# Performance work log

Measured on AMD Instinct MI355X. Metric: run time of the kernel, lower is better.

Reference implementation:

```python
import jax, jax.numpy as jnp
import numpy as np

TOP_K = 2  # init arg top_k
EPS = 1e-9


def setup_inputs() -> dict:
    key = jax.random.key(0)
    ks = jax.random.split(key, 5)
    B, L, D, E, H, G = 2, 2048, 2048, 8, 2048, 256
    s = lambda k, sh, fan: jax.random.normal(k, sh, jnp.float32) / np.sqrt(fan)
    return {
        "x": jax.random.normal(ks[0], (B, L, D), jnp.float32),
        "wg1": s(ks[1], (D, G), D),
        "wg2": s(ks[2], (G, E), G),
        "w1": s(ks[3], (E, D, H), D),
        "w2": s(ks[4], (E, H, D), H),
    }


def reference(x, wg1, wg2, w1, w2):
    B, L, D = x.shape
    xf = x.reshape(-1, D)                                  # [T, D]
    T = xf.shape[0]

    # --- top-k gating (mlp gate) ---
    logits = jax.nn.gelu(xf @ wg1) @ wg2                   # [T, E]
    probs = jax.nn.softmax(logits, axis=-1)                # [T, E]
    top_vals, top_idx = jax.lax.top_k(probs, TOP_K)        # [T, k]
    # dense gate matrix: gate weight where expert selected, else 0
    gates = jnp.zeros_like(probs).at[jnp.arange(T)[:, None], top_idx].set(top_vals)  # [T, E]

    # --- grouped expert FFN (dense-equivalent of gather/grouped-GEMM/scatter) ---
    h = jax.nn.gelu(jnp.einsum('td,edh->teh', xf, w1))     # [T, E, H]
    gh = h * gates[:, :, None]                             # fold gates in (linear in h)
    y = jnp.einsum('teh,ehd->td', gh, w2).reshape(B, L, D)

    # --- mutual-information aux loss: -H(E) + H(E|X) ---
    p_mean = probs.mean(axis=0)                            # [E]
    loss = jnp.sum(p_mean * jnp.log(p_mean + EPS)) \
         - jnp.mean(jnp.sum(probs * jnp.log(probs + EPS), axis=-1))
    return y, loss
```

## Files before the change

kernel.cpp:

```cpp
#include <hip/hip_runtime.h>

#define T_TOK 4096
#define NROWS_MAX 10240
#define MAX_TILES 40

typedef float  fv4  __attribute__((ext_vector_type(4)));
typedef __bf16 bv4  __attribute__((ext_vector_type(4)));
typedef __bf16 bv8  __attribute__((ext_vector_type(8)));

#define CTRL_OFF     0
#define ROWTOK_OFF   4096
#define ROWGATE_OFF  45056
#define TOPIDX_OFF   86016
#define TOPVAL_OFF   118784
#define G_OFF        151552
#define XB_OFF       4345856
#define W1T_OFF      21123072
#define W2T_OFF      88231936
#define HBUF_OFF     155340800

struct Ctrl {
    int   counts[8];
    float psum[8];
    float entsum;
    int   ntiles;
    int   off[8];
    int   tile_e[MAX_TILES];
    int   tile_r0[MAX_TILES];
};

__device__ __forceinline__ float gelu_f(float x) {
    float x3 = x * x * x;
    return 0.5f * x * (1.0f + tanhf(0.7978845608028654f * (x + 0.044715f * x3)));
}

__device__ __forceinline__ void g2l16(const void* gptr, void* lptr) {
    __builtin_amdgcn_global_load_lds(
        (const __attribute__((address_space(1))) void*)gptr,
        (__attribute__((address_space(3))) void*)lptr, 16, 0, 0);
}

__global__ __launch_bounds__(256) void transpose_cvt(
    const float* __restrict__ w1, const float* __restrict__ w2,
    __bf16* __restrict__ w1t, __bf16* __restrict__ w2t)
{
    int b    = blockIdx.x;
    int mat  = b >> 10;
    int tile = b & 1023;
    int trow = tile >> 5, tcol = tile & 31;
    const float* src = (mat < 8) ? (w1 + (size_t)mat * 4194304)
                                 : (w2 + (size_t)(mat - 8) * 4194304);
    __bf16* dst = (mat < 8) ? (w1t + (size_t)mat * 4194304)
                            : (w2t + (size_t)(mat - 8) * 4194304);
    __shared__ float tileS[64][65];
    int tid = threadIdx.x;
    int c = tid & 63, r4 = tid >> 6;
#pragma unroll
    for (int u = 0; u < 16; u++) {
        int rr = u * 4 + r4;
        tileS[rr][c] = src[(size_t)(trow * 64 + rr) * 2048 + tcol * 64 + c];
    }
    __syncthreads();
    int c2 = (tid & 31) * 2, r8 = tid >> 5;
#pragma unroll
    for (int u = 0; u < 8; u++) {
        int rr = u * 8 + r8;
        __bf16 v0 = (__bf16)tileS[c2][rr];
        __bf16 v1 = (__bf16)tileS[c2 + 1][rr];
        size_t o = (size_t)(tcol * 64 + rr) * 2048 + trow * 64 + c2;
        dst[o]     = v0;
        dst[o + 1] = v1;
    }
}

__global__ __launch_bounds__(256) void cvt_x_kernel(const float* __restrict__ x,
                                                    __bf16* __restrict__ xb)
{
    size_t idx = ((size_t)blockIdx.x * 256 + threadIdx.x) * 4;
    fv4 v = *(const fv4*)(x + idx);
    bv4 o;
#pragma unroll
    for (int u = 0; u < 4; u++) o[u] = (__bf16)v[u];
    *(bv4*)(xb + idx) = o;
}

__global__ __launch_bounds__(256) void gating_gemm(const float* __restrict__ x,
                                                   const float* __restrict__ wg1,
                                                   float* __restrict__ g)
{
    __shared__ float As[16][68];
    __shared__ float Bs[16][68];
    int tid = threadIdx.x;
    int tx = tid & 15, ty = tid >> 4;
    int mb = blockIdx.x, nb = blockIdx.y;
    float acc[4][4];
#pragma unroll
    for (int u = 0; u < 4; u++)
#pragma unroll
        for (int v = 0; v < 4; v++) acc[u][v] = 0.f;

    int r  = tid >> 2, kq = tid & 3;
    int kb = tid >> 4, n4 = (tid & 15) * 4;
    const float* gx = x + (size_t)(mb * 64 + r) * 2048 + kq * 4;
    const float* gw = wg1 + nb * 64 + n4;

    for (int k0 = 0; k0 < 2048; k0 += 16) {
        fv4 av = *(const fv4*)(gx + k0);
        fv4 bv = *(const fv4*)(gw + (size_t)(k0 + kb) * 256);
        __syncthreads();
#pragma unroll
        for (int u = 0; u < 4; u++) As[kq * 4 + u][r] = av[u];
        *(fv4*)&Bs[kb][n4] = bv;
        __syncthreads();
#pragma unroll
        for (int k = 0; k < 16; k++) {
            fv4 a = *(const fv4*)&As[k][ty * 4];
            fv4 b = *(const fv4*)&Bs[k][tx * 4];
#pragma unroll
            for (int u = 0; u < 4; u++)
#pragma unroll
                for (int v = 0; v < 4; v++) acc[u][v] += a[u] * b[v];
        }
    }
#pragma unroll
    for (int u = 0; u < 4; u++) {
        int row = mb * 64 + ty * 4 + u;
#pragma unroll
        for (int v = 0; v < 4; v++)
            g[(size_t)row * 256 + nb * 64 + tx * 4 + v] = gelu_f(acc[u][v]);
    }
}

__global__ __launch_bounds__(256) void gate_kernel(
    const float* __restrict__ g, const float* __restrict__ wg2,
    Ctrl* __restrict__ ctrl, int* __restrict__ topidx, float* __restrict__ topval)
{
    __shared__ float wg2s[256 * 9];
    __shared__ float psum_s[8];
    __shared__ float ent_s;
    __shared__ int   cnt_s[8];
    int tid = threadIdx.x;
    for (int i = tid; i < 2048; i += 256) {
        int k = i >> 3, e = i & 7;
        wg2s[k * 9 + e] = wg2[i];
    }
    if (tid < 8) { psum_s[tid] = 0.f; cnt_s[tid] = 0; }
    if (tid == 8) ent_s = 0.f;
    __syncthreads();

    int lane = tid & 63, wv = tid >> 6;
    int t = blockIdx.x * 4 + wv;
    fv4 g4 = *(const fv4*)&g[(size_t)t * 256 + lane * 4];
    float part[8];
#pragma unroll
    for (int e = 0; e < 8; e++) part[e] = 0.f;
#pragma unroll
    for (int u = 0; u < 4; u++) {
        int k = lane * 4 + u;
        float gv = g4[u];
#pragma unroll
        for (int e = 0; e < 8; e++) part[e] += gv * wg2s[k * 9 + e];
    }
#pragma unroll
    for (int e = 0; e < 8; e++)
        for (int off = 32; off; off >>= 1) part[e] += __shfl_xor(part[e], off);

    if (lane == 0) {
        float mx = part[0];
#pragma unroll
        for (int e = 1; e < 8; e++) mx = fmaxf(mx, part[e]);
        float p[8], Z = 0.f;
#pragma unroll
        for (int e = 0; e < 8; e++) { p[e] = expf(part[e] - mx); Z += p[e]; }
        float rz = 1.f / Z;
#pragma unroll
        for (int e = 0; e < 8; e++) p[e] *= rz;
        int i0 = 0;
#pragma unroll
        for (int e = 1; e < 8; e++) if (part[e] > part[i0]) i0 = e;
        int i1 = (i0 == 0) ? 1 : 0;
#pragma unroll
        for (int e = 0; e < 8; e++)
            if (e != i0 && part[e] > part[i1]) i1 = e;
        topidx[2 * t]     = i0;
        topidx[2 * t + 1] = i1;
        topval[2 * t]     = p[i0];
        topval[2 * t + 1] = p[i1];
        float ent = 0.f;
#pragma unroll
        for (int e = 0; e < 8; e++) ent += p[e] * logf(p[e] + 1e-9f);
#pragma unroll
        for (int e = 0; e < 8; e++) atomicAdd(&psum_s[e], p[e]);
        atomicAdd(&ent_s, ent);
        atomicAdd(&cnt_s[i0], 1);
        atomicAdd(&cnt_s[i1], 1);
    }
    __syncthreads();
    if (tid < 8)                    atomicAdd(&ctrl->psum[tid], psum_s[tid]);
    else if (tid == 8)              atomicAdd(&ctrl->entsum, ent_s);
    else if (tid >= 16 && tid < 24) atomicAdd(&ctrl->counts[tid - 16], cnt_s[tid - 16]);
}

__global__ __launch_bounds__(256) void route_kernel(
    Ctrl* __restrict__ ctrl, const int* __restrict__ topidx,
    const float* __restrict__ topval, int* __restrict__ rowtok,
    float* __restrict__ rowgate)
{
    __shared__ int cur[8];
    __shared__ int offs_s[8];
    int tid = threadIdx.x;
    if (tid == 0) {
        int off = 0, nt = 0;
        for (int e = 0; e < 8; e++) {
            offs_s[e]    = off;
            ctrl->off[e] = off;
            int c = ctrl->counts[e];
            for (int m = 0; m < c; m += 256) {
                ctrl->tile_e[nt]  = e;
                ctrl->tile_r0[nt] = off + m;
                nt++;
            }
            off += ((c + 255) >> 8) << 8;
        }
        ctrl->ntiles = nt;
    }
    if (tid < 8) cur[tid] = 0;
    __syncthreads();
    for (int t = tid; t < T_TOK; t += 256) {
#pragma unroll
        for (int k = 0; k < 2; k++) {
            int e = topidx[2 * t + k];
            int p = atomicAdd(&cur[e], 1);
            int row = offs_s[e] + p;
            rowtok[row]  = t;
            rowgate[row] = topval[2 * t + k];
        }
    }
}

template <bool IS_FFN1>
__global__ __launch_bounds__(512, 2) void gemm_grouped(
    const __bf16* __restrict__ A,
    const __bf16* __restrict__ Bt,
    const Ctrl* __restrict__ ctrl,
    const int* __restrict__ rowtok,
    const float* __restrict__ rowgate,
    __bf16* __restrict__ hbuf,
    float* __restrict__ y)
{
    int lb   = blockIdx.x;
    int tile = (lb & 7) * 5 + (lb >> 6);
    int nb   = (lb >> 3) & 7;
    if (tile >= ctrl->ntiles) return;
    int e  = ctrl->tile_e[tile];
    int r0 = ctrl->tile_r0[tile];
    const int K = 2048;

    __shared__ __bf16 As[256 * 32];
    __shared__ __bf16 Bs[256 * 32];

    int tid  = threadIdx.x;
    int lane = tid & 63, w = tid >> 6;
    int wr = w >> 1, wc = w & 1;

    int c0 = 2 * w, c1 = c0 + 1;
    int sub = lane >> 2;
    int kcg = (lane & 3) ^ ((lane >> 3) & 3);

    int rA0 = c0 * 16 + sub, rA1 = c1 * 16 + sub;
    size_t ga0, ga1;
    if constexpr (IS_FFN1) {
        ga0 = (size_t)rowtok[r0 + rA0] * K;
        ga1 = (size_t)rowtok[r0 + rA1] * K;
    } else {
        ga0 = (size_t)(r0 + rA0) * K;
        ga1 = (size_t)(r0 + rA1) * K;
    }
    const __bf16* gA0 = A + ga0 + kcg * 8;
    const __bf16* gA1 = A + ga1 + kcg * 8;
    const __bf16* gB0 = Bt + ((size_t)e * 2048 + nb * 256 + c0 * 16 + sub) * K + kcg * 8;
    const __bf16* gB1 = Bt + ((size_t)e * 2048 + nb * 256 + c1 * 16 + sub) * K + kcg * 8;
    __bf16* lA0 = &As[c0 * 512];
    __bf16* lA1 = &As[c1 * 512];
    __bf16* lB0 = &Bs[c0 * 512];
    __bf16* lB1 = &Bs[c1 * 512];

    fv4 acc[4][8];
#pragma unroll
    for (int i = 0; i < 4; i++)
#pragma unroll
        for (int j = 0; j < 8; j++) acc[i][j] = (fv4)0.0f;

    int frow = (lane & 15) * 32 + (((lane >> 4) ^ ((lane >> 1) & 3)) * 8);

    for (int k0 = 0; k0 < K; k0 += 32) {
        __syncthreads();
        g2l16(gA0, lA0);
        g2l16(gA1, lA1);
        g2l16(gB0, lB0);
        g2l16(gB1, lB1);
        gA0 += 32; gA1 += 32; gB0 += 32; gB1 += 32;
        __syncthreads();
        bv8 aF[4], bF[8];
#pragma unroll
        for (int i = 0; i < 4; i++) aF[i] = *(const bv8*)&As[(wr * 64 + i * 16) * 32 + frow];
#pragma unroll
        for (int j = 0; j < 8; j++) bF[j] = *(const bv8*)&Bs[(wc * 128 + j * 16) * 32 + frow];
#pragma unroll
        for (int i = 0; i < 4; i++)
#pragma unroll
            for (int j = 0; j < 8; j++)
                acc[i][j] = __builtin_amdgcn_mfma_f32_16x16x32_bf16(aF[i], bF[j], acc[i][j], 0, 0, 0);
    }

    int colb = nb * 256 + wc * 128 + (lane & 15);
    int rb   = r0 + wr * 64 + (lane >> 4) * 4;
#pragma unroll
    for (int i = 0; i < 4; i++) {
#pragma unroll
        for (int rr = 0; rr < 4; rr++) {
            int rg = rb + i * 16 + rr;
            if constexpr (IS_FFN1) {
                float gate = rowgate[rg];
                size_t ho = (size_t)rg * 2048;
#pragma unroll
                for (int j = 0; j < 8; j++)
                    hbuf[ho + colb + j * 16] = (__bf16)(gelu_f(acc[i][j][rr]) * gate);
            } else {
                size_t yo = (size_t)rowtok[rg] * 2048;
#pragma unroll
                for (int j = 0; j < 8; j++)
                    atomicAdd(&y[yo + colb + j * 16], acc[i][j][rr]);
            }
        }
    }
}

__global__ __launch_bounds__(64) void loss_kernel(const Ctrl* __restrict__ ctrl,
                                                  float* __restrict__ out)
{
    if (threadIdx.x == 0) {
        float a = 0.f;
#pragma unroll
        for (int e = 0; e < 8; e++) {
            float pm = ctrl->psum[e] * (1.0f / 4096.0f);
            a += pm * logf(pm + 1e-9f);
        }
        out[0] = a - ctrl->entsum * (1.0f / 4096.0f);
    }
}

extern "C" void kernel_launch(void* const* d_in, const int* in_sizes, int n_in,
                              void* d_out, int out_size, void* d_ws, size_t ws_size,
                              hipStream_t stream)
{
    const float* x   = (const float*)d_in[0];
    const float* wg1 = (const float*)d_in[1];
    const float* wg2 = (const float*)d_in[2];
    const float* w1  = (const float*)d_in[3];
    const float* w2  = (const float*)d_in[4];
    float* out = (float*)d_out;

    char* ws = (char*)d_ws;
    Ctrl*   ctrl    = (Ctrl*)(ws + CTRL_OFF);
    int*    rowtok  = (int*)(ws + ROWTOK_OFF);
    float*  rowgate = (float*)(ws + ROWGATE_OFF);
    int*    topidx  = (int*)(ws + TOPIDX_OFF);
    float*  topval  = (float*)(ws + TOPVAL_OFF);
    float*  g       = (float*)(ws + G_OFF);
    __bf16* xb      = (__bf16*)(ws + XB_OFF);
    __bf16* w1t     = (__bf16*)(ws + W1T_OFF);
    __bf16* w2t     = (__bf16*)(ws + W2T_OFF);
    __bf16* hbuf    = (__bf16*)(ws + HBUF_OFF);

    hipMemsetAsync(ws + CTRL_OFF, 0, 4096, stream);
    hipMemsetAsync(ws + ROWTOK_OFF, 0, 81920, stream);
    hipMemsetAsync(d_out, 0, (size_t)out_size * sizeof(float), stream);

    transpose_cvt<<<16384, 256, 0, stream>>>(w1, w2, w1t, w2t);
    cvt_x_kernel<<<8192, 256, 0, stream>>>(x, xb);
    gating_gemm<<<dim3(64, 4), 256, 0, stream>>>(x, wg1, g);
    gate_kernel<<<1024, 256, 0, stream>>>(g, wg2, ctrl, topidx, topval);
    route_kernel<<<1, 256, 0, stream>>>(ctrl, topidx, topval, rowtok, rowgate);
    gemm_grouped<true><<<320, 512, 0, stream>>>(xb, w1t, ctrl, rowtok, rowgate, hbuf, nullptr);
    gemm_grouped<false><<<320, 512, 0, stream>>>(hbuf, w2t, ctrl, rowtok, rowgate, nullptr, out);
    loss_kernel<<<1, 64, 0, stream>>>(ctrl, out + 8388608);
}
```

Before: 957.6 us.

## Triple-buffer LDS loads and run grouped GEMM as a persistent 256-block grid

Replaces the synchronous load-then-compute loop in the grouped expert GEMMs with a three-stage LDS ring buffer. Async global-to-LDS loads are issued two K-steps ahead, gated by vmcnt waits and a single barrier per step. The launch also moves from 320 one-tile blocks to 256 persistent blocks, each handling up to two tile items through a fixed item mapping. The aim is to hide global memory latency behind MFMA work and to reduce tail imbalance. In exchange it uses 96KB of shared memory, which may lower occupancy below two blocks per CU, and some blocks do twice the work.

```diff
diff --git a/kernel.cpp b/kernel.cpp
--- a/kernel.cpp
+++ b/kernel.cpp
@@ -238,6 +238,8 @@
     }
 }
 
+#define WAIT_VM4 0x0F74
+#define WAIT_VM0 0x0F70
 template <bool IS_FFN1>
 __global__ __launch_bounds__(512, 2) void gemm_grouped(
     const __bf16* __restrict__ A,
@@ -248,89 +250,118 @@
     __bf16* __restrict__ hbuf,
     float* __restrict__ y)
 {
-    int lb   = blockIdx.x;
-    int tile = (lb & 7) * 5 + (lb >> 6);
-    int nb   = (lb >> 3) & 7;
-    if (tile >= ctrl->ntiles) return;
-    int e  = ctrl->tile_e[tile];
-    int r0 = ctrl->tile_r0[tile];
     const int K = 2048;
-
-    __shared__ __bf16 As[256 * 32];
-    __shared__ __bf16 Bs[256 * 32];
+    __shared__ __bf16 smem[3 * 16384];
 
     int tid  = threadIdx.x;
     int lane = tid & 63, w = tid >> 6;
     int wr = w >> 1, wc = w & 1;
-
     int c0 = 2 * w, c1 = c0 + 1;
     int sub = lane >> 2;
     int kcg = (lane & 3) ^ ((lane >> 3) & 3);
-
-    int rA0 = c0 * 16 + sub, rA1 = c1 * 16 + sub;
-    size_t ga0, ga1;
-    if constexpr (IS_FFN1) {
-        ga0 = (size_t)rowtok[r0 + rA0] * K;
-        ga1 = (size_t)rowtok[r0 + rA1] * K;
-    } else {
-        ga0 = (size_t)(r0 + rA0) * K;
-        ga1 = (size_t)(r0 + rA1) * K;
-    }
-    const __bf16* gA0 = A + ga0 + kcg * 8;
-    const __bf16* gA1 = A + ga1 + kcg * 8;
-    const __bf16* gB0 = Bt + ((size_t)e * 2048 + nb * 256 + c0 * 16 + sub) * K + kcg * 8;
-    const __bf16* gB1 = Bt + ((size_t)e * 2048 + nb * 256 + c1 * 16 + sub) * K + kcg * 8;
-    __bf16* lA0 = &As[c0 * 512];
-    __bf16* lA1 = &As[c1 * 512];
-    __bf16* lB0 = &Bs[c0 * 512];
-    __bf16* lB1 = &Bs[c1 * 512];
-
-    fv4 acc[4][8];
-#pragma unroll
-    for (int i = 0; i < 4; i++)
-#pragma unroll
-        for (int j = 0; j < 8; j++) acc[i][j] = (fv4)0.0f;
-
     int frow = (lane & 15) * 32 + (((lane >> 4) ^ ((lane >> 1) & 3)) * 8);
 
-    for (int k0 = 0; k0 < K; k0 += 32) {
-        __syncthreads();
-        g2l16(gA0, lA0);
-        g2l16(gA1, lA1);
-        g2l16(gB0, lB0);
-        g2l16(gB1, lB1);
-        gA0 += 32; gA1 += 32; gB0 += 32; gB1 += 32;
-        __syncthreads();
-        bv8 aF[4], bF[8];
-#pragma unroll
-        for (int i = 0; i < 4; i++) aF[i] = *(const bv8*)&As[(wr * 64 + i * 16) * 32 + frow];
-#pragma unroll
-        for (int j = 0; j < 8; j++) bF[j] = *(const bv8*)&Bs[(wc * 128 + j * 16) * 32 + frow];
+    int ntiles = ctrl->ntiles;
+    int x = blockIdx.x & 7, s = blockIdx.x >> 3;
+
+    int items[2]; int ni = 0;
+    {
+        int i0 = x * 32 + s;
+        int tl = ((i0 >> 5) << 2) | (i0 & 3);
+        if (tl < ntiles) items[ni++] = i0;
+    }
+    if (s < 8) {
+        int i1 = 256 + x * 8 + s;
+        int tl = ((i1 >> 5) << 2) | (i1 & 3);
+        if (tl < ntiles) items[ni++] = i1;
+    }
+
+    for (int it = 0; it < ni; it++) {
+        int item = items[it];
+        int idx  = item & 31;
+        int tl   = ((item >> 5) << 2) | (idx & 3);
+        int nb   = (idx >> 2) & 7;
+        int e    = ctrl->tile_e[tl];
+        int r0   = ctrl->tile_r0[tl];
+
+        size_t ga0, ga1;
+        if constexpr (IS_FFN1) {
+            ga0 = (size_t)rowtok[r0 + c0 * 16 + sub] * K;
+            ga1 = (size_t)rowtok[r0 + c1 * 16 + sub] * K;
+        } else {
+            ga0 = (size_t)(r0 + c0 * 16 + sub) * K;
+            ga1 = (size_t)(r0 + c1 * 16 + sub) * K;
+        }
+        const __bf16* pA0 = A + ga0 + kcg * 8;
+        const __bf16* pA1 = A + ga1 + kcg * 8;
+        const __bf16* pB0 = Bt + ((size_t)e * 2048 + nb * 256 + c0 * 16 + sub) * K + kcg * 8;
+        const __bf16* pB1 = Bt + ((size_t)e * 2048 + nb * 256 + c1 * 16 + sub) * K + kcg * 8;
+
+        fv4 acc[4][8];
 #pragma unroll
         for (int i = 0; i < 4; i++)
 #pragma unroll
+            for (int j = 0; j < 8; j++) acc[i][j] = (fv4)0.0f;
+
+        __builtin_amdgcn_s_barrier();
+#pragma unroll
+        for (int pk = 0; pk < 2; pk++) {
+            __bf16* lb = smem + pk * 16384;
+            g2l16(pA0 + pk * 32, lb + c0 * 512);
+            g2l16(pA1 + pk * 32, lb + c1 * 512);
+            g2l16(pB0 + pk * 32, lb + 8192 + c0 * 512);
+            g2l16(pB1 + pk * 32, lb + 8192 + c1 * 512);
+        }
+
+        int bcur = 0;
+        for (int k = 0; k < 64; k++) {
+            if (k < 63) __builtin_amdgcn_s_waitcnt(WAIT_VM4);
+            else        __builtin_amdgcn_s_waitcnt(WAIT_VM0);
+            __builtin_amdgcn_s_barrier();
+            if (k < 62) {
+                int bnext = bcur + 32768; if (bnext >= 49152) bnext -= 49152;
+                __bf16* lb = smem + bnext;
+                int ke = (k + 2) * 32;
+                g2l16(pA0 + ke, lb + c0 * 512);
+                g2l16(pA1 + ke, lb + c1 * 512);
+                g2l16(pB0 + ke, lb + 8192 + c0 * 512);
+                g2l16(pB1 + ke, lb + 8192 + c1 * 512);
+            }
+            const __bf16* lb = smem + bcur;
+            bv8 aF[4], bF[8];
+#pragma unroll
+            for (int i = 0; i < 4; i++)
+                aF[i] = *(const bv8*)&lb[(wr * 64 + i * 16) * 32 + frow];
+#pragma unroll
             for (int j = 0; j < 8; j++)
-                acc[i][j] = __builtin_amdgcn_mfma_f32_16x16x32_bf16(aF[i], bF[j], acc[i][j], 0, 0, 0);
-    }
-
-    int colb = nb * 256 + wc * 128 + (lane & 15);
-    int rb   = r0 + wr * 64 + (lane >> 4) * 4;
-#pragma unroll
-    for (int i = 0; i < 4; i++) {
-#pragma unroll
-        for (int rr = 0; rr < 4; rr++) {
-            int rg = rb + i * 16 + rr;
-            if constexpr (IS_FFN1) {
-                float gate = rowgate[rg];
-                size_t ho = (size_t)rg * 2048;
+                bF[j] = *(const bv8*)&lb[8192 + (wc * 128 + j * 16) * 32 + frow];
+#pragma unroll
+            for (int i = 0; i < 4; i++)
 #pragma unroll
                 for (int j = 0; j < 8; j++)
-                    hbuf[ho + colb + j * 16] = (__bf16)(gelu_f(acc[i][j][rr]) * gate);
-            } else {
-                size_t yo = (size_t)rowtok[rg] * 2048;
-#pragma unroll
-                for (int j = 0; j < 8; j++)
-                    atomicAdd(&y[yo + colb + j * 16], acc[i][j][rr]);
+                    acc[i][j] = __builtin_amdgcn_mfma_f32_16x16x32_bf16(aF[i], bF[j], acc[i][j], 0, 0, 0);
+            bcur += 16384; if (bcur >= 49152) bcur -= 49152;
+        }
+
+        int colb = nb * 256 + wc * 128 + (lane & 15);
+        int rb   = r0 + wr * 64 + (lane >> 4) * 4;
+#pragma unroll
+        for (int i = 0; i < 4; i++) {
+#pragma unroll
+            for (int rr = 0; rr < 4; rr++) {
+                int rg = rb + i * 16 + rr;
+                if constexpr (IS_FFN1) {
+                    float gate = rowgate[rg];
+                    size_t ho = (size_t)rg * 2048;
+#pragma unroll
+                    for (int j = 0; j < 8; j++)
+                        hbuf[ho + colb + j * 16] = (__bf16)(gelu_f(acc[i][j][rr]) * gate);
+                } else {
+                    size_t yo = (size_t)rowtok[rg] * 2048;
+#pragma unroll
+                    for (int j = 0; j < 8; j++)
+                        atomicAdd(&y[yo + colb + j * 16], acc[i][j][rr]);
+                }
             }
         }
     }
@@ -382,7 +413,7 @@
     gating_gemm<<<dim3(64, 4), 256, 0, stream>>>(x, wg1, g);
     gate_kernel<<<1024, 256, 0, stream>>>(g, wg2, ctrl, topidx, topval);
     route_kernel<<<1, 256, 0, stream>>>(ctrl, topidx, topval, rowtok, rowgate);
-    gemm_grouped<true><<<320, 512, 0, stream>>>(xb, w1t, ctrl, rowtok, rowgate, hbuf, nullptr);
-    gemm_grouped<false><<<320, 512, 0, stream>>>(hbuf, w2t, ctrl, rowtok, rowgate, nullptr, out);
+    gemm_grouped<true><<<256, 512, 0, stream>>>(xb, w1t, ctrl, rowtok, rowgate, hbuf, nullptr);
+    gemm_grouped<false><<<256, 512, 0, stream>>>(hbuf, w2t, ctrl, rowtok, rowgate, nullptr, out);
     loss_kernel<<<1, 64, 0, stream>>>(ctrl, out + 8388608);
 }
```

Measured after the change: 871.9 us. 1.1x faster.
